# Kernel optimization log

Hardware: AMD Instinct MI355X
Metric: run time of the kernel (lower is better)

The kernel has to match this reference:

```python
import jax, jax.numpy as jnp
import numpy as np

T, I, H, C = 2048, 1024, 1024, 1000


def _lstm(x, W_ih, W_hh, b_ih, b_hh):
    # x: [T, I]; PyTorch LSTM gate order: i, f, g, o
    x_proj = x @ W_ih.T + b_ih + b_hh  # [T, 4H] input projection hoisted out of scan
    h_dim = W_hh.shape[1]

    def step(carry, xp):
        h, c = carry
        gates = xp + h @ W_hh.T  # [4H]
        i, f, g, o = jnp.split(gates, 4)
        i = jax.nn.sigmoid(i)
        f = jax.nn.sigmoid(f)
        g = jnp.tanh(g)
        o = jax.nn.sigmoid(o)
        c_new = f * c + i * g
        h_new = o * jnp.tanh(c_new)
        return (h_new, c_new), h_new

    h0 = jnp.zeros((h_dim,), x.dtype)
    (_, _), hs = jax.lax.scan(step, (h0, h0), x_proj)
    return hs  # [T, H]


def setup_inputs() -> dict:
    key = jax.random.key(0)
    ks = jax.random.split(key, 12)
    s = 1.0 / np.sqrt(H)  # torch LSTM uniform(-1/sqrt(H), 1/sqrt(H)) scale
    u = lambda k, shape: jax.random.uniform(k, shape, jnp.float32, -s, s)
    return {
        "x": jax.random.normal(ks[0], (T, I), jnp.float32),
        "W_ih_f": u(ks[1], (4 * H, I)),
        "W_hh_f": u(ks[2], (4 * H, H)),
        "b_ih_f": u(ks[3], (4 * H,)),
        "b_hh_f": u(ks[4], (4 * H,)),
        "W_ih_b": u(ks[5], (4 * H, I)),
        "W_hh_b": u(ks[6], (4 * H, H)),
        "b_ih_b": u(ks[7], (4 * H,)),
        "b_hh_b": u(ks[8], (4 * H,)),
        "fc_W": u(ks[9], (C, 2 * H)),
        "fc_b": u(ks[10], (C,)),
    }


def reference(x, W_ih_f, W_hh_f, b_ih_f, b_hh_f, W_ih_b, W_hh_b, b_ih_b, b_hh_b, fc_W, fc_b):
    h_fwd = _lstm(x, W_ih_f, W_hh_f, b_ih_f, b_hh_f)            # [T, H]
    h_bwd = _lstm(x[::-1], W_ih_b, W_hh_b, b_ih_b, b_hh_b)[::-1]  # [T, H], re-reversed
    h = jnp.concatenate([h_fwd, h_bwd], axis=-1)                  # [T, 2H]
    return h @ fc_W.T + fc_b                                      # [T, C]
```

## Files before the change

kernel.cpp:

```cpp
#include <hip/hip_runtime.h>
#include <hip/hip_bf16.h>
#include <cstdint>


typedef __fp16 h2 __attribute__((ext_vector_type(2)));
typedef __fp16 h8 __attribute__((ext_vector_type(8)));
typedef float f4 __attribute__((ext_vector_type(4)));
typedef unsigned long long u64;

#define T_LEN 2048

static __device__ __forceinline__ unsigned int packh2(float a, float b) {
  h2 r = __builtin_amdgcn_cvt_pkrtz(a, b);
  return __builtin_bit_cast(unsigned int, r);
}
static __device__ __forceinline__ float fdot2u(unsigned int a, unsigned int b, float c) {
  return __builtin_amdgcn_fdot2(__builtin_bit_cast(h2, a), __builtin_bit_cast(h2, b), c, false);
}
static __device__ __forceinline__ float sigmoidf_(float x) {
  return 1.f / (1.f + __expf(-x));
}
static __device__ __forceinline__ float tanhf_(float x) {
  float e = __expf(-2.f * fabsf(x));
  float r = (1.f - e) / (1.f + e);
  return copysignf(r, x);
}

__global__ void convert_all(const float* __restrict__ x, const float* __restrict__ wf,
                            const float* __restrict__ wb, const float* __restrict__ fcw,
                            _Float16* __restrict__ xf, _Float16* __restrict__ wff,
                            _Float16* __restrict__ wbf, _Float16* __restrict__ fcwf) {
  const size_t SX = 2097152, SW = 4194304, SFC = 2097152;
  size_t i = (size_t)blockIdx.x * 256 + threadIdx.x;
  if (i < SX) {
    xf[i] = (_Float16)x[i];
  } else if (i < SX + SW) {
    size_t j = i - SX; wff[j] = (_Float16)wf[j];
  } else if (i < SX + 2 * SW) {
    size_t j = i - SX - SW; wbf[j] = (_Float16)wb[j];
  } else if (i < SX + 2 * SW + SFC) {
    size_t j = i - SX - 2 * SW;
    int row = (int)(j >> 11), col = (int)(j & 2047);
    fcwf[j] = (row < 1000) ? (_Float16)fcw[(size_t)row * 2048 + col] : (_Float16)0.f;
  }
}

__global__ void init_state(u64* __restrict__ hc) {
  int t = threadIdx.x;
  for (int i = t; i < 2048; i += 256) hc[i] = 0ull;
}

#define LSTR 80

template <int MODE>
__global__ __launch_bounds__(256, 2) void gemm_f16(
    const _Float16* __restrict__ A, const _Float16* __restrict__ B,
    const float* __restrict__ bias1, const float* __restrict__ bias2,
    void* __restrict__ Cout, int M, int N, int K, int nout, int rev) {
  __shared__ _Float16 As[128 * LSTR];
  __shared__ _Float16 Bs[128 * LSTR];

  const int tid = threadIdx.x;
  const int ntn = N >> 7;
  const int tm = blockIdx.x / ntn, tn = blockIdx.x % ntn;
  const int wid = tid >> 6, lane = tid & 63;
  const int wr = wid >> 1, wc = wid & 1;
  const int quad = lane >> 4, l16 = lane & 15;

  const int srow = tid >> 1, seg = tid & 1;
  const int arow = rev ? (M - 1 - (tm * 128 + srow)) : (tm * 128 + srow);
  const int brow = tn * 128 + srow;

  f4 acc[4][4];
#pragma unroll
  for (int i = 0; i < 4; ++i)
#pragma unroll
    for (int j = 0; j < 4; ++j) acc[i][j] = (f4)0.f;

  for (int k0 = 0; k0 < K; k0 += 64) {
    uint4 va[4], vb[4];
    const uint4* gpa = (const uint4*)(A + (size_t)arow * K + k0 + seg * 32);
    const uint4* gpb = (const uint4*)(B + (size_t)brow * K + k0 + seg * 32);
#pragma unroll
    for (int c = 0; c < 4; ++c) va[c] = gpa[c];
#pragma unroll
    for (int c = 0; c < 4; ++c) vb[c] = gpb[c];

    __syncthreads();
    uint4* lpa = (uint4*)&As[srow * LSTR + seg * 32];
    uint4* lpb = (uint4*)&Bs[srow * LSTR + seg * 32];
#pragma unroll
    for (int c = 0; c < 4; ++c) lpa[c] = va[c];
#pragma unroll
    for (int c = 0; c < 4; ++c) lpb[c] = vb[c];
    __syncthreads();

#pragma unroll
    for (int kk = 0; kk < 64; kk += 32) {
      h8 af[4], bf[4];
#pragma unroll
      for (int i = 0; i < 4; ++i) {
        int m = wr * 64 + i * 16 + l16;
        af[i] = *(const h8*)&As[m * LSTR + kk + quad * 8];
        int n = wc * 64 + i * 16 + l16;
        bf[i] = *(const h8*)&Bs[n * LSTR + kk + quad * 8];
      }
#pragma unroll
      for (int i = 0; i < 4; ++i)
#pragma unroll
        for (int j = 0; j < 4; ++j)
          acc[i][j] = __builtin_amdgcn_mfma_f32_16x16x32_f16(af[i], bf[j], acc[i][j], 0, 0, 0);
    }
  }

  const int cm0 = tm * 128 + wr * 64, cn0 = tn * 128 + wc * 64;
#pragma unroll
  for (int i = 0; i < 4; ++i) {
#pragma unroll
    for (int j = 0; j < 4; ++j) {
      int n = cn0 + j * 16 + l16;
#pragma unroll
      for (int r = 0; r < 4; ++r) {
        int m = cm0 + i * 16 + quad * 4 + r;
        float v = acc[i][j][r];
        if (MODE == 0) {
          v += bias1[n] + bias2[n];
          ((_Float16*)Cout)[(size_t)m * N + n] = (_Float16)v;
        } else {
          if (n < nout) ((float*)Cout)[(size_t)m * nout + n] = v + bias1[n];
        }
      }
    }
  }
}

__global__ __launch_bounds__(256, 1) void lstm_rec(
    const float* __restrict__ Whh_f, const float* __restrict__ Whh_b,
    const _Float16* __restrict__ xp,
    u64* __restrict__ hc,
    _Float16* __restrict__ hhist) {
  const int tid = threadIdx.x;
  const int blk = blockIdx.x;
  const int dir = blk >> 6;
  const int ib = blk & 63;
  const int j0 = ib * 16;
  const int wv = tid >> 6;
  const int l = tid & 63;
  const int g = l >> 4;
  const int kq = l & 15;
  const int q = l & 3;
  const int wrow0 = g * 1024 + j0 + 4 * wv;

  const float* Whh = dir ? Whh_b : Whh_f;
  const _Float16* xpd = xp + (size_t)dir * (2048u * 4096u);

  __shared__ unsigned int lds_h[2][16 * 36];
  __shared__ float lds_tr[4 * 16];

  unsigned int w[4][32];
#pragma unroll
  for (int j = 0; j < 4; ++j) {
    const float* wp = Whh + (size_t)(wrow0 + j) * 1024 + kq * 64;
#pragma unroll
    for (int i = 0; i < 16; ++i) {
      float4 v = ((const float4*)wp)[i];
      w[j][2 * i] = packh2(v.x, v.y);
      w[j][2 * i + 1] = packh2(v.z, v.w);
    }
  }

  float c = 0.f;

  uint2 xv = *(const uint2*)(xpd + wrow0);
  h2 x01 = __builtin_bit_cast(h2, xv.x);
  h2 x23 = __builtin_bit_cast(h2, xv.y);
  float xf[4] = {(float)x01[0], (float)x01[1], (float)x23[0], (float)x23[1]};

  for (int t = 0; t < T_LEN; ++t) {
    const int buf = t & 1;
    unsigned d0, d1;
    {
      u64* src = hc + (((size_t)buf * 2 + dir) * 512 + 2 * tid);
      u64 a = __hip_atomic_load(&src[0], __ATOMIC_RELAXED, __HIP_MEMORY_SCOPE_AGENT);
      u64 b = __hip_atomic_load(&src[1], __ATOMIC_RELAXED, __HIP_MEMORY_SCOPE_AGENT);
      int cnt = 0;
      while ((unsigned)a != (unsigned)t || (unsigned)b != (unsigned)t) {
        if (++cnt > (1 << 12)) break;
        a = __hip_atomic_load(&src[0], __ATOMIC_RELAXED, __HIP_MEMORY_SCOPE_AGENT);
        b = __hip_atomic_load(&src[1], __ATOMIC_RELAXED, __HIP_MEMORY_SCOPE_AGENT);
      }
      d0 = (unsigned)(a >> 32);
      d1 = (unsigned)(b >> 32);
    }

    int tnx = (t + 1 < T_LEN) ? t + 1 : t;
    uint2 xn = *(const uint2*)(xpd + (size_t)tnx * 4096 + wrow0);

    *(uint2*)&lds_h[buf][(tid >> 4) * 36 + 2 * (tid & 15)] = make_uint2(d0, d1);
    __syncthreads();

    float acc0 = 0.f, acc1 = 0.f, acc2 = 0.f, acc3 = 0.f;
    const uint4* hp = (const uint4*)&lds_h[buf][kq * 36];
#pragma unroll
    for (int i = 0; i < 8; ++i) {
      uint4 hv = hp[i];
      acc0 = fdot2u(w[0][4 * i + 0], hv.x, acc0);
      acc0 = fdot2u(w[0][4 * i + 1], hv.y, acc0);
      acc0 = fdot2u(w[0][4 * i + 2], hv.z, acc0);
      acc0 = fdot2u(w[0][4 * i + 3], hv.w, acc0);
      acc1 = fdot2u(w[1][4 * i + 0], hv.x, acc1);
      acc1 = fdot2u(w[1][4 * i + 1], hv.y, acc1);
      acc1 = fdot2u(w[1][4 * i + 2], hv.z, acc1);
      acc1 = fdot2u(w[1][4 * i + 3], hv.w, acc1);
      acc2 = fdot2u(w[2][4 * i + 0], hv.x, acc2);
      acc2 = fdot2u(w[2][4 * i + 1], hv.y, acc2);
      acc2 = fdot2u(w[2][4 * i + 2], hv.z, acc2);
      acc2 = fdot2u(w[2][4 * i + 3], hv.w, acc2);
      acc3 = fdot2u(w[3][4 * i + 0], hv.x, acc3);
      acc3 = fdot2u(w[3][4 * i + 1], hv.y, acc3);
      acc3 = fdot2u(w[3][4 * i + 2], hv.z, acc3);
      acc3 = fdot2u(w[3][4 * i + 3], hv.w, acc3);
    }
#pragma unroll
    for (int m = 1; m < 16; m <<= 1) {
      acc0 += __shfl_xor(acc0, m, 64);
      acc1 += __shfl_xor(acc1, m, 64);
      acc2 += __shfl_xor(acc2, m, 64);
      acc3 += __shfl_xor(acc3, m, 64);
    }

    if (kq == 0) {
      f4 v = {acc0 + xf[0], acc1 + xf[1], acc2 + xf[2], acc3 + xf[3]};
      *(f4*)&lds_tr[wv * 16 + g * 4] = v;
    }
    float pi = lds_tr[wv * 16 + 0 + q];
    float pf = lds_tr[wv * 16 + 4 + q];
    float pg = lds_tr[wv * 16 + 8 + q];
    float po = lds_tr[wv * 16 + 12 + q];

    float ii = sigmoidf_(pi);
    float ff = sigmoidf_(pf);
    float g_ = tanhf_(pg);
    float oo = sigmoidf_(po);
    c = ff * c + ii * g_;
    float h = oo * tanhf_(c);

    float h1 = __shfl(h, 1, 64);
    float h2v = __shfl(h, 2, 64);
    float h3 = __shfl(h, 3, 64);
    if (l == 0) {
      unsigned p01 = packh2(h, h1);
      unsigned p23 = packh2(h2v, h3);
      u64 w0 = ((u64)p01 << 32) | (unsigned)(t + 1);
      u64 w1 = ((u64)p23 << 32) | (unsigned)(t + 1);
      u64* dst = hc + (((size_t)((t + 1) & 1) * 2 + dir) * 512 + (ib * 8 + 2 * wv));
      __hip_atomic_store(&dst[0], w0, __ATOMIC_RELAXED, __HIP_MEMORY_SCOPE_AGENT);
      __hip_atomic_store(&dst[1], w1, __ATOMIC_RELAXED, __HIP_MEMORY_SCOPE_AGENT);
      int tout = dir ? (T_LEN - 1 - t) : t;
      *(uint2*)&hhist[(size_t)tout * 2048 + dir * 1024 + j0 + 4 * wv] =
          make_uint2(p01, p23);
    }

    x01 = __builtin_bit_cast(h2, xn.x);
    x23 = __builtin_bit_cast(h2, xn.y);
    xf[0] = (float)x01[0]; xf[1] = (float)x01[1];
    xf[2] = (float)x23[0]; xf[3] = (float)x23[1];
  }
}

extern "C" void kernel_launch(void* const* d_in, const int* in_sizes, int n_in,
                              void* d_out, int out_size, void* d_ws, size_t ws_size,
                              hipStream_t stream) {
  (void)in_sizes; (void)n_in; (void)out_size; (void)ws_size;
  const float* x     = (const float*)d_in[0];
  const float* Wih_f = (const float*)d_in[1];
  const float* Whh_f = (const float*)d_in[2];
  const float* bih_f = (const float*)d_in[3];
  const float* bhh_f = (const float*)d_in[4];
  const float* Wih_b = (const float*)d_in[5];
  const float* Whh_b = (const float*)d_in[6];
  const float* bih_b = (const float*)d_in[7];
  const float* bhh_b = (const float*)d_in[8];
  const float* fcW   = (const float*)d_in[9];
  const float* fcb   = (const float*)d_in[10];

  char* ws = (char*)d_ws;
  _Float16* xf16   = (_Float16*)(ws + 0);
  _Float16* wih16f = (_Float16*)(ws + 4194304);
  _Float16* wih16b = (_Float16*)(ws + 12582912);
  _Float16* fcw16  = (_Float16*)(ws + 20971520);
  _Float16* xp16   = (_Float16*)(ws + 25165824);
  _Float16* hhist  = (_Float16*)(ws + 58720256);
  u64*      hc     = (u64*)     (ws + 67108864);

  const size_t SX = 2097152, SW = 4194304, SFC = 2097152;
  const size_t total_cvt = SX + 2 * SW + SFC;

  convert_all<<<dim3((unsigned)((total_cvt + 255) / 256)), 256, 0, stream>>>(
      x, Wih_f, Wih_b, fcW, xf16, wih16f, wih16b, fcw16);
  init_state<<<1, 256, 0, stream>>>(hc);

  gemm_f16<0><<<dim3(512), 256, 0, stream>>>(xf16, wih16f, bih_f, bhh_f,
                                             (void*)xp16, 2048, 4096, 1024, 4096, 0);
  gemm_f16<0><<<dim3(512), 256, 0, stream>>>(xf16, wih16b, bih_b, bhh_b,
                                             (void*)(xp16 + (size_t)2048 * 4096),
                                             2048, 4096, 1024, 4096, 1);

  lstm_rec<<<dim3(128), 256, 0, stream>>>(Whh_f, Whh_b, xp16, hc, hhist);

  gemm_f16<1><<<dim3(128), 256, 0, stream>>>(hhist, fcw16, fcb, nullptr,
                                             d_out, 2048, 1024, 2048, 1000, 0);
}
```

Before: 3.736 ms.

## Spread LSTM recurrence over 256 blocks and vectorize fp16 conversion

The persistent recurrence kernel now runs 256 workgroups, each owning 8 hidden units instead of 16, so every thread holds 2 weight rows rather than 4 and does half the dot-product work per step. The LDS transpose used to gather gate pre-activations is replaced by cross-lane shuffles, which removes an LDS round trip from the serial step. The input conversion kernel now handles four floats per thread with vector loads and stores. In exchange, each step needs more workgroups to finish and publish their flags, so cross-block synchronisation traffic and polling latency rise, and all 256 blocks must be co-resident for the spin-wait scheme to work.

```diff
diff --git a/kernel.cpp b/kernel.cpp
--- a/kernel.cpp
+++ b/kernel.cpp
@@ -31,17 +31,24 @@
                             _Float16* __restrict__ xf, _Float16* __restrict__ wff,
                             _Float16* __restrict__ wbf, _Float16* __restrict__ fcwf) {
   const size_t SX = 2097152, SW = 4194304, SFC = 2097152;
-  size_t i = (size_t)blockIdx.x * 256 + threadIdx.x;
+  size_t i = ((size_t)blockIdx.x * 256 + threadIdx.x) * 4;
   if (i < SX) {
-    xf[i] = (_Float16)x[i];
+    float4 v = *(const float4*)(x + i);
+    *(uint2*)(xf + i) = make_uint2(packh2(v.x, v.y), packh2(v.z, v.w));
   } else if (i < SX + SW) {
-    size_t j = i - SX; wff[j] = (_Float16)wf[j];
+    size_t j = i - SX;
+    float4 v = *(const float4*)(wf + j);
+    *(uint2*)(wff + j) = make_uint2(packh2(v.x, v.y), packh2(v.z, v.w));
   } else if (i < SX + 2 * SW) {
-    size_t j = i - SX - SW; wbf[j] = (_Float16)wb[j];
+    size_t j = i - SX - SW;
+    float4 v = *(const float4*)(wb + j);
+    *(uint2*)(wbf + j) = make_uint2(packh2(v.x, v.y), packh2(v.z, v.w));
   } else if (i < SX + 2 * SW + SFC) {
     size_t j = i - SX - 2 * SW;
     int row = (int)(j >> 11), col = (int)(j & 2047);
-    fcwf[j] = (row < 1000) ? (_Float16)fcw[(size_t)row * 2048 + col] : (_Float16)0.f;
+    float4 v = make_float4(0.f, 0.f, 0.f, 0.f);
+    if (row < 1000) v = *(const float4*)(fcw + (size_t)row * 2048 + col);
+    *(uint2*)(fcwf + j) = make_uint2(packh2(v.x, v.y), packh2(v.z, v.w));
   }
 }
 
@@ -141,40 +148,38 @@
     _Float16* __restrict__ hhist) {
   const int tid = threadIdx.x;
   const int blk = blockIdx.x;
-  const int dir = blk >> 6;
-  const int ib = blk & 63;
-  const int j0 = ib * 16;
+  const int dir = blk >> 7;
+  const int ib = blk & 127;
+  const int j0 = ib * 8;
   const int wv = tid >> 6;
   const int l = tid & 63;
   const int g = l >> 4;
   const int kq = l & 15;
-  const int q = l & 3;
-  const int wrow0 = g * 1024 + j0 + 4 * wv;
+  const int q = l & 1;
+  const int wrow0 = g * 1024 + j0 + 2 * wv;
 
   const float* Whh = dir ? Whh_b : Whh_f;
   const _Float16* xpd = xp + (size_t)dir * (2048u * 4096u);
 
   __shared__ unsigned int lds_h[2][16 * 36];
-  __shared__ float lds_tr[4 * 16];
-
-  unsigned int w[4][32];
-#pragma unroll
-  for (int j = 0; j < 4; ++j) {
-    const float* wp = Whh + (size_t)(wrow0 + j) * 1024 + kq * 64;
+
+  unsigned int w[2][32];
+#pragma unroll
+  for (int r = 0; r < 2; ++r) {
+    const float* wp = Whh + (size_t)(wrow0 + r) * 1024 + kq * 64;
 #pragma unroll
     for (int i = 0; i < 16; ++i) {
       float4 v = ((const float4*)wp)[i];
-      w[j][2 * i] = packh2(v.x, v.y);
-      w[j][2 * i + 1] = packh2(v.z, v.w);
+      w[r][2 * i] = packh2(v.x, v.y);
+      w[r][2 * i + 1] = packh2(v.z, v.w);
     }
   }
 
   float c = 0.f;
 
-  uint2 xv = *(const uint2*)(xpd + wrow0);
-  h2 x01 = __builtin_bit_cast(h2, xv.x);
-  h2 x23 = __builtin_bit_cast(h2, xv.y);
-  float xf[4] = {(float)x01[0], (float)x01[1], (float)x23[0], (float)x23[1]};
+  unsigned xv = *(const unsigned*)(xpd + wrow0);
+  h2 xh = __builtin_bit_cast(h2, xv);
+  float xf0 = (float)xh[0], xf1 = (float)xh[1];
 
   for (int t = 0; t < T_LEN; ++t) {
     const int buf = t & 1;
@@ -194,12 +199,12 @@
     }
 
     int tnx = (t + 1 < T_LEN) ? t + 1 : t;
-    uint2 xn = *(const uint2*)(xpd + (size_t)tnx * 4096 + wrow0);
+    unsigned xn = *(const unsigned*)(xpd + (size_t)tnx * 4096 + wrow0);
 
     *(uint2*)&lds_h[buf][(tid >> 4) * 36 + 2 * (tid & 15)] = make_uint2(d0, d1);
     __syncthreads();
 
-    float acc0 = 0.f, acc1 = 0.f, acc2 = 0.f, acc3 = 0.f;
+    float acc0 = 0.f, acc1 = 0.f;
     const uint4* hp = (const uint4*)&lds_h[buf][kq * 36];
 #pragma unroll
     for (int i = 0; i < 8; ++i) {
@@ -212,31 +217,18 @@
       acc1 = fdot2u(w[1][4 * i + 1], hv.y, acc1);
       acc1 = fdot2u(w[1][4 * i + 2], hv.z, acc1);
       acc1 = fdot2u(w[1][4 * i + 3], hv.w, acc1);
-      acc2 = fdot2u(w[2][4 * i + 0], hv.x, acc2);
-      acc2 = fdot2u(w[2][4 * i + 1], hv.y, acc2);
-      acc2 = fdot2u(w[2][4 * i + 2], hv.z, acc2);
-      acc2 = fdot2u(w[2][4 * i + 3], hv.w, acc2);
-      acc3 = fdot2u(w[3][4 * i + 0], hv.x, acc3);
-      acc3 = fdot2u(w[3][4 * i + 1], hv.y, acc3);
-      acc3 = fdot2u(w[3][4 * i + 2], hv.z, acc3);
-      acc3 = fdot2u(w[3][4 * i + 3], hv.w, acc3);
     }
 #pragma unroll
     for (int m = 1; m < 16; m <<= 1) {
       acc0 += __shfl_xor(acc0, m, 64);
       acc1 += __shfl_xor(acc1, m, 64);
-      acc2 += __shfl_xor(acc2, m, 64);
-      acc3 += __shfl_xor(acc3, m, 64);
-    }
-
-    if (kq == 0) {
-      f4 v = {acc0 + xf[0], acc1 + xf[1], acc2 + xf[2], acc3 + xf[3]};
-      *(f4*)&lds_tr[wv * 16 + g * 4] = v;
-    }
-    float pi = lds_tr[wv * 16 + 0 + q];
-    float pf = lds_tr[wv * 16 + 4 + q];
-    float pg = lds_tr[wv * 16 + 8 + q];
-    float po = lds_tr[wv * 16 + 12 + q];
+    }
+
+    float val = (q ? acc1 + xf1 : acc0 + xf0);
+    float pi = __shfl(val, 0 + q, 64);
+    float pf = __shfl(val, 16 + q, 64);
+    float pg = __shfl(val, 32 + q, 64);
+    float po = __shfl(val, 48 + q, 64);
 
     float ii = sigmoidf_(pi);
     float ff = sigmoidf_(pf);
@@ -246,25 +238,18 @@
     float h = oo * tanhf_(c);
 
     float h1 = __shfl(h, 1, 64);
-    float h2v = __shfl(h, 2, 64);
-    float h3 = __shfl(h, 3, 64);
     if (l == 0) {
-      unsigned p01 = packh2(h, h1);
-      unsigned p23 = packh2(h2v, h3);
-      u64 w0 = ((u64)p01 << 32) | (unsigned)(t + 1);
-      u64 w1 = ((u64)p23 << 32) | (unsigned)(t + 1);
-      u64* dst = hc + (((size_t)((t + 1) & 1) * 2 + dir) * 512 + (ib * 8 + 2 * wv));
-      __hip_atomic_store(&dst[0], w0, __ATOMIC_RELAXED, __HIP_MEMORY_SCOPE_AGENT);
-      __hip_atomic_store(&dst[1], w1, __ATOMIC_RELAXED, __HIP_MEMORY_SCOPE_AGENT);
+      unsigned hh = packh2(h, h1);
+      u64 word = ((u64)hh << 32) | (unsigned)(t + 1);
+      u64* dst = hc + (((size_t)((t + 1) & 1) * 2 + dir) * 512 + (ib * 4 + wv));
+      __hip_atomic_store(dst, word, __ATOMIC_RELAXED, __HIP_MEMORY_SCOPE_AGENT);
       int tout = dir ? (T_LEN - 1 - t) : t;
-      *(uint2*)&hhist[(size_t)tout * 2048 + dir * 1024 + j0 + 4 * wv] =
-          make_uint2(p01, p23);
-    }
-
-    x01 = __builtin_bit_cast(h2, xn.x);
-    x23 = __builtin_bit_cast(h2, xn.y);
-    xf[0] = (float)x01[0]; xf[1] = (float)x01[1];
-    xf[2] = (float)x23[0]; xf[3] = (float)x23[1];
+      *(unsigned*)&hhist[(size_t)tout * 2048 + dir * 1024 + j0 + 2 * wv] = hh;
+    }
+
+    xh = __builtin_bit_cast(h2, xn);
+    xf0 = (float)xh[0];
+    xf1 = (float)xh[1];
   }
 }
 
@@ -296,7 +281,7 @@
   const size_t SX = 2097152, SW = 4194304, SFC = 2097152;
   const size_t total_cvt = SX + 2 * SW + SFC;
 
-  convert_all<<<dim3((unsigned)((total_cvt + 255) / 256)), 256, 0, stream>>>(
+  convert_all<<<dim3((unsigned)(total_cvt / 4 / 256)), 256, 0, stream>>>(
       x, Wih_f, Wih_b, fcW, xf16, wih16f, wih16b, fcw16);
   init_state<<<1, 256, 0, stream>>>(hc);
 
@@ -306,7 +291,7 @@
                                              (void*)(xp16 + (size_t)2048 * 4096),
                                              2048, 4096, 1024, 4096, 1);
 
-  lstm_rec<<<dim3(128), 256, 0, stream>>>(Whh_f, Whh_b, xp16, hc, hhist);
+  lstm_rec<<<dim3(256), 256, 0, stream>>>(Whh_f, Whh_b, xp16, hc, hhist);
 
   gemm_f16<1><<<dim3(128), 256, 0, stream>>>(hhist, fcw16, fcb, nullptr,
                                              d_out, 2048, 1024, 2048, 1000, 0);
```

Result: slower. 7.173 ms (+92.0%).
